# Kernel optimization log

Measured on AMD Instinct MI355X. Metric: run time of the kernel, lower is better.

Reference implementation:

```python
import jax, jax.numpy as jnp
import numpy as np
from functools import partial

# ---- constants mirroring init_kwargs ----
T, B, J, I = 1024, 32, 128, 512
KD = 16              # max_delay (dilated kernel size)
THETA = 1.0          # threshold
SIG = 0.5            # delay.SIG, frozen (requires_grad=False)
ALPHA = 5.0          # ATan surrogate alpha
EPS = 1e-5           # BatchNorm eps

# ---- ATan surrogate spike (spikingjelly): fwd = heaviside, bwd = atan grad ----
@jax.custom_vjp
def atan_spike(x):
    return (x >= 0).astype(x.dtype)

def _atan_fwd(x):
    return atan_spike(x), x

def _atan_bwd(x, g):
    return (g * (ALPHA / 2.0) / (1.0 + (jnp.pi / 2.0 * ALPHA * x) ** 2),)

atan_spike.defvjp(_atan_fwd, _atan_bwd)

def _dcls_kernel(w, P):
    # DCLS1d 'gauss' version, kernel_count=1: gaussian bump centered at P + KD//2,
    # normalized over the kernel axis, scaled by weight. w,P: (I,J) -> (I,J,KD)
    c = P + KD // 2
    k = jnp.arange(KD, dtype=w.dtype)                        # (KD,)
    g = jnp.exp(-0.5 * ((k[None, None, :] - c[:, :, None]) / SIG) ** 2)
    g = g / (g.sum(-1, keepdims=True) + 1e-7)
    return w[:, :, None] * g                                  # (I,J,KD)

def setup_inputs() -> dict:
    key = jax.random.key(0)
    ks = jax.random.split(key, 6)
    x = jax.random.normal(ks[0], (T, B, J), dtype=jnp.float32)
    # kaiming_uniform_ fan_in = J*1 -> bound = sqrt(6/fan_in)
    bound = float(np.sqrt(6.0 / J))
    delay_w = jax.random.uniform(ks[1], (I, J), jnp.float32, -bound, bound)
    # P ~ U(-max_delay//2, max_delay//2), then clamped (already in range)
    delay_P = jax.random.uniform(ks[2], (I, J), jnp.float32, -(KD // 2), KD // 2)
    beta = jax.random.uniform(ks[3], (I,), jnp.float32, 0.0, 1.0)
    bn_gamma = jnp.ones((I,), jnp.float32)
    bn_beta = jnp.zeros((I,), jnp.float32)
    U0 = jax.random.uniform(ks[4], (B, I), jnp.float32)       # RandomBatchwiseInit(0,1)
    return {"x": x, "delay_w": delay_w, "delay_P": delay_P, "beta": beta,
            "bn_gamma": bn_gamma, "bn_beta": bn_beta, "U0": U0}

def reference(x, delay_w, delay_P, beta, bn_gamma, bn_beta, U0):
    # --- delayed conv: (T,B,J) -> (B,J,T) -> left-pad KD-1 -> conv1d -> (T,B,I) ---
    xb = jnp.transpose(x, (1, 2, 0))                          # (B,J,T)
    xb = jnp.pad(xb, ((0, 0), (0, 0), (KD - 1, 0)))           # (B,J,T+KD-1)
    kern = _dcls_kernel(delay_w, delay_P)                     # (I,J,KD)
    y = jax.lax.conv_general_dilated(
        xb, kern, window_strides=(1,), padding='VALID',
        dimension_numbers=('NCH', 'OIH', 'NCH'))              # (B,I,T)
    y = jnp.transpose(y, (2, 0, 1))                           # (T,B,I)

    # --- BatchNorm1d over reshaped (T*B, I, 1): stats over T*B per channel ---
    yf = y.reshape(T * B, I)
    mean = yf.mean(axis=0)
    var = yf.var(axis=0)
    yf = (yf - mean) * jax.lax.rsqrt(var + EPS) * bn_gamma + bn_beta
    y = yf.reshape(T, B, I)

    # --- soft-reset LIF scan (NOTE: original passes RAW beta, not sigmoid(beta)) ---
    def step(carry, xt):
        Ut, St = carry
        Ut = beta * (Ut - THETA * St) + (1.0 - beta) * xt
        St = atan_spike(Ut - THETA)
        return (Ut, St), St

    S0 = jnp.zeros_like(U0)
    _, o = jax.lax.scan(step, (U0, S0), y)                    # (T,B,I)
    return o
```

## Files before the change

kernel.cpp:

```cpp
#include <hip/hip_runtime.h>

#define TT 1024
#define NB 32
#define NJ 128
#define NI 512
#define KD 16
#define LVL 1048576

typedef short bf16x8 __attribute__((ext_vector_type(8)));
typedef float floatx4 __attribute__((ext_vector_type(4)));

struct S3 { short h, m, l; };

__device__ __forceinline__ S3 split3(float v) {
    S3 o;
    unsigned hb = __float_as_uint(v) & 0xFFFF0000u;
    float hf = __uint_as_float(hb);
    float r1 = v - hf;
    unsigned mb = __float_as_uint(r1) & 0xFFFF0000u;
    float mf = __uint_as_float(mb);
    float r2 = r1 - mf;
    unsigned lb = __float_as_uint(r2) & 0xFFFF0000u;
    o.h = (short)(hb >> 16);
    o.m = (short)(mb >> 16);
    o.l = (short)(lb >> 16);
    return o;
}

__global__ __launch_bounds__(256) void dcls_kern(const float* __restrict__ w,
                                                 const float* __restrict__ P,
                                                 short* __restrict__ WF) {
    int idx = blockIdx.x * 256 + threadIdx.x;
    int j = idx & (NJ - 1);
    int i = idx >> 7;
    float wv = w[i * NJ + j];
    float c  = P[i * NJ + j] + (float)(KD / 2);
    float g[KD];
    float s = 0.f;
#pragma unroll
    for (int k = 0; k < KD; ++k) {
        float u = (float)k - c;
        g[k] = expf(-2.0f * u * u);
        s += g[k];
    }
    float inv = wv / (s + 1e-7f);
    size_t base = (size_t)(i >> 4) * 32768 + (size_t)(j >> 3) * 128 + (i & 15) * 8 + (j & 7);
#pragma unroll
    for (int d = 0; d < KD; ++d) {
        S3 sp = split3(g[(KD - 1) - d] * inv);
        size_t off = base + (size_t)d * 2048;
        WF[off]           = sp.h;
        WF[off + LVL]     = sp.m;
        WF[off + 2 * LVL] = sp.l;
    }
}

__global__ __launch_bounds__(256, 2) void conv_mfma(const float* __restrict__ x,
                                                    const short* __restrict__ WF,
                                                    float* __restrict__ y) {
    __shared__ __align__(16) short PA[2][128][64];
    __shared__ __align__(16) short PL[2][128][64];

    const int t0 = blockIdx.x * 128;
    const int i0 = blockIdx.y * 128;
    const int b  = blockIdx.z;
    const int tid = threadIdx.x;

    const int ch   = tid & 3;
    const int rw2  = tid >> 2;
    const int l    = tid & 63;
    const int wid  = tid >> 6;
    const int lr16 = l & 15;
    const int kb   = l >> 4;
    const int wm   = wid >> 1;
    const int wn   = wid & 1;

    const short* pnf[4];
#pragma unroll
    for (int nf = 0; nf < 4; ++nf) {
        int ig = (i0 + wn * 64 + nf * 16) >> 4;
        pnf[nf] = WF + (size_t)ig * 32768 + l * 8;
    }

    floatx4 acc[4][4];
#pragma unroll
    for (int mf = 0; mf < 4; ++mf)
#pragma unroll
        for (int nf = 0; nf < 4; ++nf)
#pragma unroll
            for (int e = 0; e < 4; ++e) acc[mf][nf][e] = 0.f;

    float4 ga[2][2];
    bf16x8 W0h[4], W0m[4], W0l[4], W1h[4], W1m[4], W1l[4];

#define LOADW(K, H, M, L_) {                                                    \
    int koff = ((((K) >> 2) * 16 + ((K) & 3) * 4)) * 128;                       \
    _Pragma("unroll") for (int nf = 0; nf < 4; ++nf) {                          \
        const short* p = pnf[nf] + koff;                                        \
        H[nf]  = *(const bf16x8*)(p);                                           \
        M[nf]  = *(const bf16x8*)(p + LVL);                                     \
        L_[nf] = *(const bf16x8*)(p + 2 * LVL); } }

#define LOADX(K) {                                                              \
    int dn = (K) >> 2, j0n = ((K) & 3) << 5;                                    \
    _Pragma("unroll") for (int s = 0; s < 2; ++s) {                             \
        int r = rw2 + s * 64;                                                   \
        int t = t0 + r - dn;                                                    \
        float4 z4 = make_float4(0.f, 0.f, 0.f, 0.f);                            \
        ga[s][0] = z4; ga[s][1] = z4;                                           \
        if (t >= 0) {                                                           \
            const float* ax = x + ((size_t)t * NB + b) * NJ + j0n + ch * 8;     \
            ga[s][0] = *(const float4*)ax;                                      \
            ga[s][1] = *(const float4*)(ax + 4); } } }

#define STAGEW(BUFA, BUFL) {                                                    \
    _Pragma("unroll") for (int s = 0; s < 2; ++s) {                             \
        int r = rw2 + s * 64;                                                   \
        int key = r & 7;                                                        \
        char* rowA = (char*)(BUFA) + r * 128;                                   \
        char* rowL = (char*)(BUFL) + r * 128;                                   \
        S3 a0 = split3(ga[s][0].x), a1 = split3(ga[s][0].y),                    \
           a2 = split3(ga[s][0].z), a3 = split3(ga[s][0].w),                    \
           a4 = split3(ga[s][1].x), a5 = split3(ga[s][1].y),                    \
           a6 = split3(ga[s][1].z), a7 = split3(ga[s][1].w);                    \
        bf16x8 h8, m8, l8;                                                      \
        h8[0]=a0.h; h8[1]=a1.h; h8[2]=a2.h; h8[3]=a3.h;                         \
        h8[4]=a4.h; h8[5]=a5.h; h8[6]=a6.h; h8[7]=a7.h;                         \
        m8[0]=a0.m; m8[1]=a1.m; m8[2]=a2.m; m8[3]=a3.m;                         \
        m8[4]=a4.m; m8[5]=a5.m; m8[6]=a6.m; m8[7]=a7.m;                         \
        l8[0]=a0.l; l8[1]=a1.l; l8[2]=a2.l; l8[3]=a3.l;                         \
        l8[4]=a4.l; l8[5]=a5.l; l8[6]=a6.l; l8[7]=a7.l;                         \
        *(bf16x8*)(rowA + ((ch ^ key) * 16))       = h8;                        \
        *(bf16x8*)(rowA + (((ch + 4) ^ key) * 16)) = m8;                        \
        *(bf16x8*)(rowL + ((ch ^ key) * 16))       = l8; } }

#define DOMFMA(BUFA, BUFL, CH, CM, CL) {                                        \
    _Pragma("unroll") for (int mf = 0; mf < 4; ++mf) {                          \
        int row = wm * 64 + mf * 16 + lr16;                                     \
        int key = row & 7;                                                      \
        const char* rowA = (const char*)(BUFA) + row * 128;                     \
        const char* rowL = (const char*)(BUFL) + row * 128;                     \
        bf16x8 ah = *(const bf16x8*)(rowA + ((kb ^ key) * 16));                 \
        bf16x8 am = *(const bf16x8*)(rowA + (((kb + 4) ^ key) * 16));           \
        bf16x8 al = *(const bf16x8*)(rowL + ((kb ^ key) * 16));                 \
        _Pragma("unroll") for (int nf = 0; nf < 4; ++nf)                        \
            acc[mf][nf] = __builtin_amdgcn_mfma_f32_16x16x32_bf16(ah, CH[nf], acc[mf][nf], 0, 0, 0); \
        _Pragma("unroll") for (int nf = 0; nf < 4; ++nf)                        \
            acc[mf][nf] = __builtin_amdgcn_mfma_f32_16x16x32_bf16(ah, CM[nf], acc[mf][nf], 0, 0, 0); \
        _Pragma("unroll") for (int nf = 0; nf < 4; ++nf)                        \
            acc[mf][nf] = __builtin_amdgcn_mfma_f32_16x16x32_bf16(am, CH[nf], acc[mf][nf], 0, 0, 0); \
        _Pragma("unroll") for (int nf = 0; nf < 4; ++nf)                        \
            acc[mf][nf] = __builtin_amdgcn_mfma_f32_16x16x32_bf16(am, CM[nf], acc[mf][nf], 0, 0, 0); \
        _Pragma("unroll") for (int nf = 0; nf < 4; ++nf)                        \
            acc[mf][nf] = __builtin_amdgcn_mfma_f32_16x16x32_bf16(ah, CL[nf], acc[mf][nf], 0, 0, 0); \
        _Pragma("unroll") for (int nf = 0; nf < 4; ++nf)                        \
            acc[mf][nf] = __builtin_amdgcn_mfma_f32_16x16x32_bf16(al, CH[nf], acc[mf][nf], 0, 0, 0); \
    } }

    LOADX(0)
    STAGEW(PA[0], PL[0])
    LOADX(1)
    LOADW(0, W0h, W0m, W0l)
    __syncthreads();

#pragma unroll 1
    for (int kk = 0; kk < 64; kk += 2) {
        if (kk + 1 < 64) { STAGEW(PA[1], PL[1]) }
        if (kk + 2 < 64) { LOADX(kk + 2) }
        if (kk + 1 < 64) { LOADW(kk + 1, W1h, W1m, W1l) }
        DOMFMA(PA[0], PL[0], W0h, W0m, W0l)
        __syncthreads();
        if (kk + 2 < 64) { STAGEW(PA[0], PL[0]) }
        if (kk + 3 < 64) { LOADX(kk + 3) }
        if (kk + 2 < 64) { LOADW(kk + 2, W0h, W0m, W0l) }
        if (kk + 1 < 64) { DOMFMA(PA[1], PL[1], W1h, W1m, W1l) }
        __syncthreads();
    }
#undef LOADW
#undef LOADX
#undef STAGEW
#undef DOMFMA

#pragma unroll
    for (int mf = 0; mf < 4; ++mf)
#pragma unroll
        for (int nf = 0; nf < 4; ++nf) {
            int ic = i0 + wn * 64 + nf * 16 + lr16;
#pragma unroll
            for (int q = 0; q < 4; ++q) {
                int t = t0 + wm * 64 + mf * 16 + kb * 4 + q;
                y[((size_t)t * NB + b) * NI + ic] = acc[mf][nf][q];
            }
        }
}

__global__ __launch_bounds__(256) void red1(const float* __restrict__ y,
                                            float* __restrict__ part) {
    int r0 = blockIdx.x * 128;
    int c  = threadIdx.x;
    float s0 = 0.f, q0 = 0.f, s1 = 0.f, q1 = 0.f;
#pragma unroll 4
    for (int r = 0; r < 128; ++r) {
        float v0 = y[(size_t)(r0 + r) * NI + c];
        float v1 = y[(size_t)(r0 + r) * NI + c + 256];
        s0 += v0; q0 = fmaf(v0, v0, q0);
        s1 += v1; q1 = fmaf(v1, v1, q1);
    }
    part[blockIdx.x * NI + c]            = s0;
    part[blockIdx.x * NI + c + 256]      = s1;
    part[256 * NI + blockIdx.x * NI + c]       = q0;
    part[256 * NI + blockIdx.x * NI + c + 256] = q1;
}

__global__ __launch_bounds__(512) void red2(const float* __restrict__ part,
                                            const float* __restrict__ gamma,
                                            const float* __restrict__ bbeta,
                                            float* __restrict__ sb) {
    int c = threadIdx.x;
    double s = 0.0, q = 0.0;
#pragma unroll 8
    for (int p = 0; p < 256; ++p) {
        s += (double)part[p * NI + c];
        q += (double)part[256 * NI + p * NI + c];
    }
    double mean = s / 32768.0;
    double var  = q / 32768.0 - mean * mean;
    double scale = (double)gamma[c] / sqrt(var + 1e-5);
    sb[c]      = (float)scale;
    sb[NI + c] = (float)((double)bbeta[c] - mean * scale);
}

__global__ __launch_bounds__(64) void scan_kern(float* __restrict__ y,
                                                const float* __restrict__ sb,
                                                const float* __restrict__ beta,
                                                const float* __restrict__ U0) {
    int g = blockIdx.x * 64 + threadIdx.x;
    int i = g & (NI - 1);
    float scale = sb[i];
    float bias  = sb[NI + i];
    float bet = beta[i];
    float omb = 1.f - bet;
    float u = U0[g];
    float s = 0.f;
    float* yp = y + g;

    float A[32], Bv[32];
#pragma unroll
    for (int r = 0; r < 32; ++r) A[r] = yp[(size_t)r * 16384];

    for (int t0 = 0; t0 < TT; t0 += 64) {
#pragma unroll
        for (int r = 0; r < 32; ++r) Bv[r] = yp[(size_t)(t0 + 32 + r) * 16384];
#pragma unroll
        for (int r = 0; r < 32; ++r) {
            float z = fmaf(A[r], scale, bias);
            u = fmaf(bet, u - s, omb * z);
            s = (u >= 1.f) ? 1.f : 0.f;
            yp[(size_t)(t0 + r) * 16384] = s;
        }
        if (t0 + 64 < TT) {
#pragma unroll
            for (int r = 0; r < 32; ++r) A[r] = yp[(size_t)(t0 + 64 + r) * 16384];
        }
#pragma unroll
        for (int r = 0; r < 32; ++r) {
            float z = fmaf(Bv[r], scale, bias);
            u = fmaf(bet, u - s, omb * z);
            s = (u >= 1.f) ? 1.f : 0.f;
            yp[(size_t)(t0 + 32 + r) * 16384] = s;
        }
    }
}

extern "C" void kernel_launch(void* const* d_in, const int* in_sizes, int n_in,
                              void* d_out, int out_size, void* d_ws, size_t ws_size,
                              hipStream_t stream) {
    const float* x       = (const float*)d_in[0];
    const float* delay_w = (const float*)d_in[1];
    const float* delay_P = (const float*)d_in[2];
    const float* beta    = (const float*)d_in[3];
    const float* bn_g    = (const float*)d_in[4];
    const float* bn_b    = (const float*)d_in[5];
    const float* U0      = (const float*)d_in[6];
    float* y = (float*)d_out;

    short* WF   = (short*)d_ws;
    float* part = (float*)d_ws;
    float* sb   = (float*)d_ws + 2 * 256 * NI;

    dcls_kern<<<dim3(NI * NJ / 256), dim3(256), 0, stream>>>(delay_w, delay_P, WF);
    conv_mfma<<<dim3(TT / 128, NI / 128, NB), dim3(256), 0, stream>>>(x, WF, y);
    red1<<<dim3(TT * NB / 128), dim3(256), 0, stream>>>(y, part);
    red2<<<dim3(1), dim3(512), 0, stream>>>(part, bn_g, bn_b, sb);
    scan_kern<<<dim3(NB * NI / 64), dim3(64), 0, stream>>>(y, sb, beta, U0);
}
```

Measured before the change: 368.6 us.

## Enlarge conv tile to 256x256 with 512 threads and single-buffered LDS

Grows the conv_mfma block tile from 128x128 to 256x256 (t by i) with 8 waves, each computing an 8x4 grid of MFMA fragments. This doubles per-wave accumulator reuse of the LDS A-fragments and global weight loads, cutting the redundant traffic per output. In exchange it drops the LDS double buffering and the weight-register prefetch: each k-step now does two syncs, stages, then loads weights right before the MFMAs. That exposes load latency and leaves four times fewer blocks (128 x 32 grid reduced to 4x2x32 = 256 blocks), so occupancy and CU fill may suffer.

```diff
diff --git a/kernel.cpp b/kernel.cpp
--- a/kernel.cpp
+++ b/kernel.cpp
@@ -55,25 +55,25 @@
     }
 }
 
-__global__ __launch_bounds__(256, 2) void conv_mfma(const float* __restrict__ x,
+__global__ __launch_bounds__(512, 2) void conv_mfma(const float* __restrict__ x,
                                                     const short* __restrict__ WF,
                                                     float* __restrict__ y) {
-    __shared__ __align__(16) short PA[2][128][64];
-    __shared__ __align__(16) short PL[2][128][64];
-
-    const int t0 = blockIdx.x * 128;
-    const int i0 = blockIdx.y * 128;
+    __shared__ __align__(16) short PA[256][64];
+    __shared__ __align__(16) short PL[256][64];
+
+    const int t0 = blockIdx.x * 256;
+    const int i0 = blockIdx.y * 256;
     const int b  = blockIdx.z;
     const int tid = threadIdx.x;
 
     const int ch   = tid & 3;
-    const int rw2  = tid >> 2;
+    const int rw   = tid >> 2;
     const int l    = tid & 63;
-    const int wid  = tid >> 6;
+    const int wv   = tid >> 6;
     const int lr16 = l & 15;
     const int kb   = l >> 4;
-    const int wm   = wid >> 1;
-    const int wn   = wid & 1;
+    const int wm   = wv >> 2;
+    const int wn   = wv & 3;
 
     const short* pnf[4];
 #pragma unroll
@@ -82,30 +82,29 @@
         pnf[nf] = WF + (size_t)ig * 32768 + l * 8;
     }
 
-    floatx4 acc[4][4];
-#pragma unroll
-    for (int mf = 0; mf < 4; ++mf)
+    floatx4 acc[8][4];
+#pragma unroll
+    for (int mf = 0; mf < 8; ++mf)
 #pragma unroll
         for (int nf = 0; nf < 4; ++nf)
 #pragma unroll
             for (int e = 0; e < 4; ++e) acc[mf][nf][e] = 0.f;
 
     float4 ga[2][2];
-    bf16x8 W0h[4], W0m[4], W0l[4], W1h[4], W1m[4], W1l[4];
-
-#define LOADW(K, H, M, L_) {                                                    \
+    bf16x8 Wh[4], Wm[4], Wl[4];
+
+#define LOADW(K) {                                                              \
     int koff = ((((K) >> 2) * 16 + ((K) & 3) * 4)) * 128;                       \
     _Pragma("unroll") for (int nf = 0; nf < 4; ++nf) {                          \
         const short* p = pnf[nf] + koff;                                        \
-        H[nf]  = *(const bf16x8*)(p);                                           \
-        M[nf]  = *(const bf16x8*)(p + LVL);                                     \
-        L_[nf] = *(const bf16x8*)(p + 2 * LVL); } }
+        Wh[nf] = *(const bf16x8*)(p);                                           \
+        Wm[nf] = *(const bf16x8*)(p + LVL);                                     \
+        Wl[nf] = *(const bf16x8*)(p + 2 * LVL); } }
 
 #define LOADX(K) {                                                              \
     int dn = (K) >> 2, j0n = ((K) & 3) << 5;                                    \
     _Pragma("unroll") for (int s = 0; s < 2; ++s) {                             \
-        int r = rw2 + s * 64;                                                   \
-        int t = t0 + r - dn;                                                    \
+        int t = t0 + rw + s * 128 - dn;                                         \
         float4 z4 = make_float4(0.f, 0.f, 0.f, 0.f);                            \
         ga[s][0] = z4; ga[s][1] = z4;                                           \
         if (t >= 0) {                                                           \
@@ -113,12 +112,12 @@
             ga[s][0] = *(const float4*)ax;                                      \
             ga[s][1] = *(const float4*)(ax + 4); } } }
 
-#define STAGEW(BUFA, BUFL) {                                                    \
+#define STAGEW() {                                                              \
     _Pragma("unroll") for (int s = 0; s < 2; ++s) {                             \
-        int r = rw2 + s * 64;                                                   \
+        int r = rw + s * 128;                                                   \
         int key = r & 7;                                                        \
-        char* rowA = (char*)(BUFA) + r * 128;                                   \
-        char* rowL = (char*)(BUFL) + r * 128;                                   \
+        char* rowA = (char*)PA + r * 128;                                       \
+        char* rowL = (char*)PL + r * 128;                                       \
         S3 a0 = split3(ga[s][0].x), a1 = split3(ga[s][0].y),                    \
            a2 = split3(ga[s][0].z), a3 = split3(ga[s][0].w),                    \
            a4 = split3(ga[s][1].x), a5 = split3(ga[s][1].y),                    \
@@ -134,47 +133,39 @@
         *(bf16x8*)(rowA + (((ch + 4) ^ key) * 16)) = m8;                        \
         *(bf16x8*)(rowL + ((ch ^ key) * 16))       = l8; } }
 
-#define DOMFMA(BUFA, BUFL, CH, CM, CL) {                                        \
-    _Pragma("unroll") for (int mf = 0; mf < 4; ++mf) {                          \
-        int row = wm * 64 + mf * 16 + lr16;                                     \
+#define DOMFMA() {                                                              \
+    _Pragma("unroll") for (int mf = 0; mf < 8; ++mf) {                          \
+        int row = wm * 128 + mf * 16 + lr16;                                    \
         int key = row & 7;                                                      \
-        const char* rowA = (const char*)(BUFA) + row * 128;                     \
-        const char* rowL = (const char*)(BUFL) + row * 128;                     \
+        const char* rowA = (const char*)PA + row * 128;                         \
+        const char* rowL = (const char*)PL + row * 128;                         \
         bf16x8 ah = *(const bf16x8*)(rowA + ((kb ^ key) * 16));                 \
         bf16x8 am = *(const bf16x8*)(rowA + (((kb + 4) ^ key) * 16));           \
         bf16x8 al = *(const bf16x8*)(rowL + ((kb ^ key) * 16));                 \
         _Pragma("unroll") for (int nf = 0; nf < 4; ++nf)                        \
-            acc[mf][nf] = __builtin_amdgcn_mfma_f32_16x16x32_bf16(ah, CH[nf], acc[mf][nf], 0, 0, 0); \
-        _Pragma("unroll") for (int nf = 0; nf < 4; ++nf)                        \
-            acc[mf][nf] = __builtin_amdgcn_mfma_f32_16x16x32_bf16(ah, CM[nf], acc[mf][nf], 0, 0, 0); \
-        _Pragma("unroll") for (int nf = 0; nf < 4; ++nf)                        \
-            acc[mf][nf] = __builtin_amdgcn_mfma_f32_16x16x32_bf16(am, CH[nf], acc[mf][nf], 0, 0, 0); \
-        _Pragma("unroll") for (int nf = 0; nf < 4; ++nf)                        \
-            acc[mf][nf] = __builtin_amdgcn_mfma_f32_16x16x32_bf16(am, CM[nf], acc[mf][nf], 0, 0, 0); \
-        _Pragma("unroll") for (int nf = 0; nf < 4; ++nf)                        \
-            acc[mf][nf] = __builtin_amdgcn_mfma_f32_16x16x32_bf16(ah, CL[nf], acc[mf][nf], 0, 0, 0); \
-        _Pragma("unroll") for (int nf = 0; nf < 4; ++nf)                        \
-            acc[mf][nf] = __builtin_amdgcn_mfma_f32_16x16x32_bf16(al, CH[nf], acc[mf][nf], 0, 0, 0); \
+            acc[mf][nf] = __builtin_amdgcn_mfma_f32_16x16x32_bf16(ah, Wh[nf], acc[mf][nf], 0, 0, 0); \
+        _Pragma("unroll") for (int nf = 0; nf < 4; ++nf)                        \
+            acc[mf][nf] = __builtin_amdgcn_mfma_f32_16x16x32_bf16(ah, Wm[nf], acc[mf][nf], 0, 0, 0); \
+        _Pragma("unroll") for (int nf = 0; nf < 4; ++nf)                        \
+            acc[mf][nf] = __builtin_amdgcn_mfma_f32_16x16x32_bf16(am, Wh[nf], acc[mf][nf], 0, 0, 0); \
+        _Pragma("unroll") for (int nf = 0; nf < 4; ++nf)                        \
+            acc[mf][nf] = __builtin_amdgcn_mfma_f32_16x16x32_bf16(am, Wm[nf], acc[mf][nf], 0, 0, 0); \
+        _Pragma("unroll") for (int nf = 0; nf < 4; ++nf)                        \
+            acc[mf][nf] = __builtin_amdgcn_mfma_f32_16x16x32_bf16(ah, Wl[nf], acc[mf][nf], 0, 0, 0); \
+        _Pragma("unroll") for (int nf = 0; nf < 4; ++nf)                        \
+            acc[mf][nf] = __builtin_amdgcn_mfma_f32_16x16x32_bf16(al, Wh[nf], acc[mf][nf], 0, 0, 0); \
     } }
 
     LOADX(0)
-    STAGEW(PA[0], PL[0])
-    LOADX(1)
-    LOADW(0, W0h, W0m, W0l)
-    __syncthreads();
 
 #pragma unroll 1
-    for (int kk = 0; kk < 64; kk += 2) {
-        if (kk + 1 < 64) { STAGEW(PA[1], PL[1]) }
-        if (kk + 2 < 64) { LOADX(kk + 2) }
-        if (kk + 1 < 64) { LOADW(kk + 1, W1h, W1m, W1l) }
-        DOMFMA(PA[0], PL[0], W0h, W0m, W0l)
+    for (int kk = 0; kk < 64; ++kk) {
         __syncthreads();
-        if (kk + 2 < 64) { STAGEW(PA[0], PL[0]) }
-        if (kk + 3 < 64) { LOADX(kk + 3) }
-        if (kk + 2 < 64) { LOADW(kk + 2, W0h, W0m, W0l) }
-        if (kk + 1 < 64) { DOMFMA(PA[1], PL[1], W1h, W1m, W1l) }
+        STAGEW()
         __syncthreads();
+        if (kk + 1 < 64) { LOADX(kk + 1) }
+        LOADW(kk)
+        DOMFMA()
     }
 #undef LOADW
 #undef LOADX
@@ -182,13 +173,13 @@
 #undef DOMFMA
 
 #pragma unroll
-    for (int mf = 0; mf < 4; ++mf)
+    for (int mf = 0; mf < 8; ++mf)
 #pragma unroll
         for (int nf = 0; nf < 4; ++nf) {
             int ic = i0 + wn * 64 + nf * 16 + lr16;
 #pragma unroll
             for (int q = 0; q < 4; ++q) {
-                int t = t0 + wm * 64 + mf * 16 + kb * 4 + q;
+                int t = t0 + wm * 128 + mf * 16 + kb * 4 + q;
                 y[((size_t)t * NB + b) * NI + ic] = acc[mf][nf][q];
             }
         }
@@ -289,7 +280,7 @@
     float* sb   = (float*)d_ws + 2 * 256 * NI;
 
     dcls_kern<<<dim3(NI * NJ / 256), dim3(256), 0, stream>>>(delay_w, delay_P, WF);
-    conv_mfma<<<dim3(TT / 128, NI / 128, NB), dim3(256), 0, stream>>>(x, WF, y);
+    conv_mfma<<<dim3(TT / 256, NI / 256, NB), dim3(512), 0, stream>>>(x, WF, y);
     red1<<<dim3(TT * NB / 128), dim3(256), 0, stream>>>(y, part);
     red2<<<dim3(1), dim3(512), 0, stream>>>(part, bn_g, bn_b, sb);
     scan_kern<<<dim3(NB * NI / 64), dim3(64), 0, stream>>>(y, sb, beta, U0);
```

New measurement: 357.4 us. 3.0% less time.
